# Performance work log

Measured on AMD Instinct MI355X. Metric: run time of the kernel, lower is better.

The kernel has to match this reference:

```python
import jax, jax.numpy as jnp
import numpy as np

WEIGHT_CE = 1.0
WEIGHT_DICE = 1.0
EPS = 1e-10
SMOOTH = 1e-5


def setup_inputs() -> dict:
    key = jax.random.key(0)
    k1, k2 = jax.random.split(key)
    B, N, H, W, D = 2, 8, 128, 128, 128
    logits = jax.random.normal(k1, (B, N, H, W, D), dtype=jnp.float32)
    pred = jax.nn.softmax(logits, axis=1)  # module expects softmaxed preds
    target = jax.random.randint(k2, (B, 1, H, W, D), 0, N, dtype=jnp.int32)
    return {"pred": pred, "target": target}


def reference(pred, target):
    # pred: (B, N, H, W, D) softmax probs; target: (B, 1, H, W, D) int labels
    B, N = pred.shape[0], pred.shape[1]
    t = target[:, 0]  # (B, H, W, D)

    # --- CE part (faithful to the original's cross-batch one-hot bug) ---
    # loss[b2, hwd] = -sum_b sum_c 1[t[b2,hwd]==c] * log(pred[b,c,hwd]+eps)
    logp_sum = jnp.sum(jnp.log(pred + EPS), axis=0)  # (N, H, W, D)
    gathered = jnp.take_along_axis(
        jnp.broadcast_to(logp_sum[None], (B,) + logp_sum.shape),
        t[:, None], axis=1)[:, 0]  # (B, H, W, D)
    celoss = -jnp.mean(gathered) / B

    # --- MONAI DiceLoss(softmax=False, to_onehot_y=True), defaults ---
    oh = (t[:, None] == jnp.arange(N, dtype=t.dtype)[None, :, None, None, None]).astype(pred.dtype)  # (B,N,H,W,D)
    inter = jnp.sum(oh * pred, axis=(2, 3, 4))   # (B, N)
    ground_o = jnp.sum(oh, axis=(2, 3, 4))       # (B, N)
    pred_o = jnp.sum(pred, axis=(2, 3, 4))       # (B, N)
    dice = jnp.mean(1.0 - (2.0 * inter + SMOOTH) / (ground_o + pred_o + SMOOTH))

    return WEIGHT_CE * celoss + WEIGHT_DICE * dice
```

## Files before the change

### kernel.cpp

```cpp
#include <hip/hip_runtime.h>

#define S_VOX (128*128*128)
#define QV (S_VOX/4)
#define EPSF 1e-10f
#define SMOOTHF 1e-5f

#define NACC 49

__device__ __forceinline__ float wave_reduce(float v) {
#pragma unroll
    for (int off = 32; off > 0; off >>= 1)
        v += __shfl_down(v, off, 64);
    return v;
}

__global__ __launch_bounds__(256) void dice_main(const float* __restrict__ pred,
                                                 const int* __restrict__ tgt,
                                                 float* __restrict__ ws) {
    const int b   = blockIdx.x & 1;
    const int bid = blockIdx.x >> 1;
    const int nbb = gridDim.x >> 1;

    const float4* p4   = (const float4*)pred + (size_t)b * 8u * (size_t)QV;
    const int4*   town = (const int4*)tgt + (size_t)b * (size_t)QV;
    const int4*   toth = (const int4*)tgt + (size_t)(1 - b) * (size_t)QV;

    float ce = 0.f;
    float inter[8], po[8];
    int   gc[8];
#pragma unroll
    for (int n = 0; n < 8; n++) { inter[n] = 0.f; po[n] = 0.f; gc[n] = 0; }

    const int tid0   = bid * blockDim.x + threadIdx.x;
    const int stride = nbb * blockDim.x;

    for (int q = tid0; q < QV; q += stride) {
        const int4 t0 = town[q];
        const int4 t1 = toth[q];
        float so0 = 0.f, so1 = 0.f, so2 = 0.f, so3 = 0.f;
        float st0 = 0.f, st1 = 0.f, st2 = 0.f, st3 = 0.f;
#pragma unroll
        for (int n = 0; n < 8; n++) {
            const float4 p = p4[(size_t)n * QV + q];
            po[n] += (p.x + p.y) + (p.z + p.w);

#define SLOT(pv, ta, tb, so, st)                                        \
            {                                                           \
                const bool m0 = ((ta) == n);                            \
                const bool m1 = ((tb) == n);                            \
                const float v0 = m0 ? (pv) : 0.f;                       \
                inter[n] += v0;                                         \
                so += v0;                                               \
                st += m1 ? (pv) : 0.f;                                  \
                gc[n] += (int)m0;                                       \
            }
            SLOT(p.x, t0.x, t1.x, so0, st0)
            SLOT(p.y, t0.y, t1.y, so1, st1)
            SLOT(p.z, t0.z, t1.z, so2, st2)
            SLOT(p.w, t0.w, t1.w, so3, st3)
#undef SLOT
        }
        ce += __logf(so0 + EPSF) + __logf(st0 + EPSF);
        ce += __logf(so1 + EPSF) + __logf(st1 + EPSF);
        ce += __logf(so2 + EPSF) + __logf(st2 + EPSF);
        ce += __logf(so3 + EPSF) + __logf(st3 + EPSF);
    }

    __shared__ float red[4][25];
    const int lane = threadIdx.x & 63;
    const int wave = threadIdx.x >> 6;

    float acc[25];
    acc[0] = ce;
#pragma unroll
    for (int n = 0; n < 8; n++) {
        acc[1 + n]  = inter[n];
        acc[9 + n]  = po[n];
        acc[17 + n] = (float)gc[n];
    }
#pragma unroll
    for (int i = 0; i < 25; i++) {
        float v = wave_reduce(acc[i]);
        if (lane == 0) red[wave][i] = v;
    }
    __syncthreads();

    const int i = threadIdx.x;
    if (i < 25) {
        float s = red[0][i] + red[1][i] + red[2][i] + red[3][i];
        int dst;
        if (i == 0)       dst = 0;
        else if (i <= 8)  dst = 1  + b * 8 + (i - 1);
        else if (i <= 16) dst = 33 + b * 8 + (i - 9);
        else              dst = 17 + b * 8 + (i - 17);
        atomicAdd(&ws[dst], s);
    }
}

__global__ void dice_finalize(const float* __restrict__ ws, float* __restrict__ out) {
    const int i = threadIdx.x;
    float term = 0.f;
    if (i < 16) {
        float inter = ws[1 + i];
        float g     = ws[17 + i];
        float p     = ws[33 + i];
        term = 1.0f - (2.0f * inter + SMOOTHF) / (g + p + SMOOTHF);
    }
    term = wave_reduce(term);
    if (i == 0) {
        float celoss = -ws[0] / (4.0f * (float)S_VOX);
        out[0] = celoss + term * (1.0f / 16.0f);
    }
}

extern "C" void kernel_launch(void* const* d_in, const int* in_sizes, int n_in,
                              void* d_out, int out_size, void* d_ws, size_t ws_size,
                              hipStream_t stream) {
    const float* pred = (const float*)d_in[0];
    const int*   tgt  = (const int*)d_in[1];
    float* ws  = (float*)d_ws;
    float* out = (float*)d_out;

    hipMemsetAsync(ws, 0, NACC * sizeof(float), stream);
    dice_main<<<2048, 256, 0, stream>>>(pred, tgt, ws);
    dice_finalize<<<1, 64, 0, stream>>>(ws, out);
}
```

Before: 223.3 us.

## Split work per (batch, class) plane and compute log per element

Each block now handles one contiguous chunk of a single (batch, class) plane instead of looping over all eight classes per voxel. The CE term becomes a per-element log weighted by target matches rather than a log of the gathered probability. This cuts register pressure and gives contiguous streaming per block. In exchange, both target arrays are re-read once per class (8x more target traffic) and the log count rises from 8 to 32 per quad.

```diff
diff --git a/kernel.cpp b/kernel.cpp
--- a/kernel.cpp
+++ b/kernel.cpp
@@ -2,6 +2,8 @@
 
 #define S_VOX (128*128*128)
 #define QV (S_VOX/4)
+#define BLOCKS_PER_PLANE 128
+#define CHUNK_Q (QV / BLOCKS_PER_PLANE)
 #define EPSF 1e-10f
 #define SMOOTHF 1e-5f
 
@@ -17,82 +19,57 @@
 __global__ __launch_bounds__(256) void dice_main(const float* __restrict__ pred,
                                                  const int* __restrict__ tgt,
                                                  float* __restrict__ ws) {
-    const int b   = blockIdx.x & 1;
-    const int bid = blockIdx.x >> 1;
-    const int nbb = gridDim.x >> 1;
+    const int plane = blockIdx.x >> 7;
+    const int chunk = blockIdx.x & 127;
+    const int b = plane >> 3;
+    const int n = plane & 7;
 
-    const float4* p4   = (const float4*)pred + (size_t)b * 8u * (size_t)QV;
-    const int4*   town = (const int4*)tgt + (size_t)b * (size_t)QV;
-    const int4*   toth = (const int4*)tgt + (size_t)(1 - b) * (size_t)QV;
+    const float4* p4 = (const float4*)pred + (size_t)plane * QV + (size_t)chunk * CHUNK_Q;
+    const int4*   ta = (const int4*)tgt + (size_t)b * QV        + (size_t)chunk * CHUNK_Q;
+    const int4*   tb = (const int4*)tgt + (size_t)(1 - b) * QV  + (size_t)chunk * CHUNK_Q;
 
-    float ce = 0.f;
-    float inter[8], po[8];
-    int   gc[8];
-#pragma unroll
-    for (int n = 0; n < 8; n++) { inter[n] = 0.f; po[n] = 0.f; gc[n] = 0; }
+    float po = 0.f, inter = 0.f, ce = 0.f;
+    int gc = 0;
 
-    const int tid0   = bid * blockDim.x + threadIdx.x;
-    const int stride = nbb * blockDim.x;
-
-    for (int q = tid0; q < QV; q += stride) {
-        const int4 t0 = town[q];
-        const int4 t1 = toth[q];
-        float so0 = 0.f, so1 = 0.f, so2 = 0.f, so3 = 0.f;
-        float st0 = 0.f, st1 = 0.f, st2 = 0.f, st3 = 0.f;
-#pragma unroll
-        for (int n = 0; n < 8; n++) {
-            const float4 p = p4[(size_t)n * QV + q];
-            po[n] += (p.x + p.y) + (p.z + p.w);
-
-#define SLOT(pv, ta, tb, so, st)                                        \
-            {                                                           \
-                const bool m0 = ((ta) == n);                            \
-                const bool m1 = ((tb) == n);                            \
-                const float v0 = m0 ? (pv) : 0.f;                       \
-                inter[n] += v0;                                         \
-                so += v0;                                               \
-                st += m1 ? (pv) : 0.f;                                  \
-                gc[n] += (int)m0;                                       \
-            }
-            SLOT(p.x, t0.x, t1.x, so0, st0)
-            SLOT(p.y, t0.y, t1.y, so1, st1)
-            SLOT(p.z, t0.z, t1.z, so2, st2)
-            SLOT(p.w, t0.w, t1.w, so3, st3)
+#pragma unroll 4
+    for (int i = threadIdx.x; i < CHUNK_Q; i += 256) {
+        const float4 p  = p4[i];
+        const int4   t0 = ta[i];
+        const int4   t1 = tb[i];
+        po += (p.x + p.y) + (p.z + p.w);
+#define SLOT(pv, u, v)                                          \
+        {                                                       \
+            const int m0 = ((u) == n);                          \
+            const int m1 = ((v) == n);                          \
+            inter += m0 ? (pv) : 0.f;                           \
+            gc    += m0;                                        \
+            ce    += (float)(m0 + m1) * __logf((pv) + EPSF);    \
+        }
+        SLOT(p.x, t0.x, t1.x)
+        SLOT(p.y, t0.y, t1.y)
+        SLOT(p.z, t0.z, t1.z)
+        SLOT(p.w, t0.w, t1.w)
 #undef SLOT
-        }
-        ce += __logf(so0 + EPSF) + __logf(st0 + EPSF);
-        ce += __logf(so1 + EPSF) + __logf(st1 + EPSF);
-        ce += __logf(so2 + EPSF) + __logf(st2 + EPSF);
-        ce += __logf(so3 + EPSF) + __logf(st3 + EPSF);
     }
 
-    __shared__ float red[4][25];
+    __shared__ float red[4][4];
     const int lane = threadIdx.x & 63;
     const int wave = threadIdx.x >> 6;
-
-    float acc[25];
-    acc[0] = ce;
+    float acc[4] = { ce, inter, (float)gc, po };
 #pragma unroll
-    for (int n = 0; n < 8; n++) {
-        acc[1 + n]  = inter[n];
-        acc[9 + n]  = po[n];
-        acc[17 + n] = (float)gc[n];
-    }
-#pragma unroll
-    for (int i = 0; i < 25; i++) {
+    for (int i = 0; i < 4; i++) {
         float v = wave_reduce(acc[i]);
         if (lane == 0) red[wave][i] = v;
     }
     __syncthreads();
-
-    const int i = threadIdx.x;
-    if (i < 25) {
-        float s = red[0][i] + red[1][i] + red[2][i] + red[3][i];
+    if (threadIdx.x < 4) {
+        const int i = threadIdx.x;
+        const float s = red[0][i] + red[1][i] + red[2][i] + red[3][i];
         int dst;
-        if (i == 0)       dst = 0;
-        else if (i <= 8)  dst = 1  + b * 8 + (i - 1);
-        else if (i <= 16) dst = 33 + b * 8 + (i - 9);
-        else              dst = 17 + b * 8 + (i - 17);
+        if (i == 0)      dst = 0;
+        else if (i == 1) dst = 1  + plane;
+        else if (i == 2) dst = 17 + plane;
+        else             dst = 33 + plane;
         atomicAdd(&ws[dst], s);
     }
 }
@@ -122,6 +99,6 @@
     float* out = (float*)d_out;
 
     hipMemsetAsync(ws, 0, NACC * sizeof(float), stream);
-    dice_main<<<2048, 256, 0, stream>>>(pred, tgt, ws);
+    dice_main<<<16 * BLOCKS_PER_PLANE, 256, 0, stream>>>(pred, tgt, ws);
     dice_finalize<<<1, 64, 0, stream>>>(ws, out);
 }
```

Result: slower. 230.6 us (+3.3%).
